# Kernel tuning notes

Measured on AMD Instinct MI355X. Metric: run time of the kernel, lower is better.

Reference implementation:

```python
import jax, jax.numpy as jnp
import numpy as np

N_NODES = 100000
N_EDGES = 1600000
HID = 128
N_GRAPHS = 512
MAX_Z = 1000
NODE_VOCAB = 200000
OUT = 2
BN_EPS = 1e-5


def setup_inputs() -> dict:
    key = jax.random.key(0)
    ks = jax.random.split(key, 20)

    def w(k, shape, fan_in):
        return jax.random.normal(k, shape, dtype=jnp.float32) / np.sqrt(fan_in)

    inp = {
        "num_nodes": N_NODES,
        "z": jax.random.randint(ks[0], (N_NODES,), 0, MAX_Z),
        "edge_index": jax.random.randint(ks[1], (2, N_EDGES), 0, N_NODES),
        "batch": jnp.sort(jax.random.randint(ks[2], (N_NODES,), 0, N_GRAPHS)),
        "node_id": jax.random.randint(ks[3], (N_NODES,), 0, NODE_VOCAB),
        # parameters
        "z_emb": jax.random.normal(ks[4], (MAX_Z, HID), dtype=jnp.float32) * 0.02,
        "node_emb": jax.random.normal(ks[5], (NODE_VOCAB, HID), dtype=jnp.float32) * 0.02,
        "W0": w(ks[6], (2 * HID, HID), 2 * HID), "b0": jnp.zeros((HID,), jnp.float32),
        "W1": w(ks[7], (HID, HID), HID), "b1": jnp.zeros((HID,), jnp.float32),
        "W2": w(ks[8], (HID, HID), HID), "b2": jnp.zeros((HID,), jnp.float32),
        "mlp_W1": w(ks[9], (HID, HID), HID), "mlp_b1": jnp.zeros((HID,), jnp.float32),
        "bn_gamma": jnp.ones((HID,), jnp.float32), "bn_beta": jnp.zeros((HID,), jnp.float32),
        "mlp_W2": w(ks[10], (HID, OUT), HID), "mlp_b2": jnp.zeros((OUT,), jnp.float32),
    }
    return inp


def _gin_conv(x, src, dst, W, b, num_nodes):
    # GINConv(eps=0): out_i = Linear(x_i + sum_{j->i} x_j)
    agg = jax.ops.segment_sum(x[src], dst, num_segments=num_nodes)
    return (x + agg) @ W + b


def reference(num_nodes, z, edge_index, batch, node_id,
              z_emb, node_emb, W0, b0, W1, b1, W2, b2,
              mlp_W1, mlp_b1, bn_gamma, bn_beta, mlp_W2, mlp_b2):
    src, dst = edge_index[0], edge_index[1]
    # node features: concat(z_embedding(z), node_embedding(node_id)) -> [N, 2H]
    x = jnp.concatenate([z_emb[z], node_emb[node_id]], axis=1)

    x = jax.nn.relu(_gin_conv(x, src, dst, W0, b0, num_nodes))  # [N, H]
    x = jax.nn.relu(_gin_conv(x, src, dst, W1, b1, num_nodes))
    x = _gin_conv(x, src, dst, W2, b2, num_nodes)  # last conv: no relu

    # global mean pool over graphs
    sums = jax.ops.segment_sum(x, batch, num_segments=N_GRAPHS)  # [G, H]
    counts = jax.ops.segment_sum(jnp.ones((num_nodes,), x.dtype), batch,
                                 num_segments=N_GRAPHS)
    pooled = sums / jnp.maximum(counts, 1.0)[:, None]

    # MLP([H, H, OUT]): Linear -> BatchNorm(eval, identity stats) -> ReLU -> Linear
    h = pooled @ mlp_W1 + mlp_b1
    h = h * (bn_gamma / np.sqrt(1.0 + BN_EPS)) + bn_beta
    h = jax.nn.relu(h)
    return h @ mlp_W2 + mlp_b2  # [G, OUT]
```

## Files before the change

kernel.cpp:

```cpp
#include <hip/hip_runtime.h>

#define NN 100000
#define NE 1600000
#define HID 128
#define NG 512
#define MAXZ 1000
#define NBK 256
#define BK_S 391
#define TILE_E 4096

typedef unsigned short u16;
typedef unsigned int u32;
typedef __attribute__((ext_vector_type(8))) short bf16x8;
typedef __attribute__((ext_vector_type(4))) float f32x4;

__device__ __forceinline__ u16 bf16r(float x) {
    u32 u = __float_as_uint(x);
    u32 r = (u + 0x7fffu + ((u >> 16) & 1u)) >> 16;
    return (u16)r;
}
__device__ __forceinline__ float bflo(u32 u) { return __uint_as_float(u << 16); }
__device__ __forceinline__ float bfhi(u32 u) { return __uint_as_float(u & 0xffff0000u); }

#define ACC8(v) { \
    acc[0] += bflo((v).x); acc[1] += bfhi((v).x); \
    acc[2] += bflo((v).y); acc[3] += bfhi((v).y); \
    acc[4] += bflo((v).z); acc[5] += bfhi((v).z); \
    acc[6] += bflo((v).w); acc[7] += bfhi((v).w); }

__global__ __launch_bounds__(256) void bucket_count_kernel(const int* __restrict__ dst,
                                                           int* __restrict__ bcount) {
    __shared__ int lh[NBK];
    int t = threadIdx.x;
    lh[t] = 0;
    __syncthreads();
    int stride = gridDim.x * 256;
    for (int i = blockIdx.x * 256 + t; i < NE; i += stride)
        atomicAdd(&lh[dst[i] / BK_S], 1);
    __syncthreads();
    int v = lh[t];
    if (v) atomicAdd(&bcount[t], v);
}

__global__ __launch_bounds__(NBK) void scan_nbk_kernel(const int* __restrict__ bcount,
                                                       int* __restrict__ boff,
                                                       int* __restrict__ gcursor) {
    __shared__ int buf[NBK];
    int t = threadIdx.x;
    int v = bcount[t];
    buf[t] = v;
    __syncthreads();
    for (int d = 1; d < NBK; d <<= 1) {
        int add = (t >= d) ? buf[t - d] : 0;
        __syncthreads();
        buf[t] += add;
        __syncthreads();
    }
    int excl = buf[t] - v;
    boff[t] = excl;
    gcursor[t] = excl;
    if (t == NBK - 1) boff[NBK] = buf[NBK - 1];
}

__global__ __launch_bounds__(256) void pair_scatter_kernel(const int* __restrict__ src,
                                                           const int* __restrict__ dst,
                                                           int* __restrict__ gcursor,
                                                           u32* __restrict__ pairs) {
    __shared__ int cnt[NBK];
    __shared__ int base[NBK];
    int t = threadIdx.x;
    long tile0 = (long)blockIdx.x * TILE_E;
    cnt[t] = 0;
    __syncthreads();
    u32 val[16], br[16];
#pragma unroll
    for (int i = 0; i < 16; ++i) {
        long idx = tile0 + i * 256 + t;
        val[i] = 0xFFFFFFFFu;
        if (idx < NE) {
            int d = dst[idx];
            int b = d / BK_S;
            int r = atomicAdd(&cnt[b], 1);
            val[i] = ((u32)(d - b * BK_S) << 17) | (u32)src[idx];
            br[i] = ((u32)b << 12) | (u32)r;
        }
    }
    __syncthreads();
    int c = cnt[t];
    if (c) base[t] = atomicAdd(&gcursor[t], c);
    __syncthreads();
#pragma unroll
    for (int i = 0; i < 16; ++i) {
        if (val[i] != 0xFFFFFFFFu) {
            u32 b = br[i] >> 12, r = br[i] & 0xFFFu;
            pairs[base[b] + r] = val[i];
        }
    }
}

__global__ __launch_bounds__(256) void bucket_build_kernel(const u32* __restrict__ pairs,
                                                           const int* __restrict__ boff,
                                                           int* __restrict__ off,
                                                           int* __restrict__ csr) {
    __shared__ int lh[BK_S];
    __shared__ int ts[256];
    int b = blockIdx.x, t = threadIdx.x;
    int base = boff[b], end = boff[b + 1];
    int node0 = b * BK_S;
    for (int i = t; i < BK_S; i += 256) lh[i] = 0;
    __syncthreads();
    for (int j = base + t; j < end; j += 256)
        atomicAdd(&lh[pairs[j] >> 17], 1);
    __syncthreads();
    int i0 = t * 2, i1 = t * 2 + 1;
    int c0 = (i0 < BK_S) ? lh[i0] : 0;
    int c1 = (i1 < BK_S) ? lh[i1] : 0;
    int s = c0 + c1;
    ts[t] = s;
    __syncthreads();
    for (int d = 1; d < 256; d <<= 1) {
        int add = (t >= d) ? ts[t - d] : 0;
        __syncthreads();
        ts[t] += add;
        __syncthreads();
    }
    int e0 = base + ts[t] - s;
    int e1 = e0 + c0;
    if (i0 < BK_S) { lh[i0] = e0; int n = node0 + i0; if (n < NN) off[n] = e0; }
    if (i1 < BK_S) { lh[i1] = e1; int n = node0 + i1; if (n < NN) off[n] = e1; }
    if (b == 0 && t == 0) off[NN] = NE;
    __syncthreads();
    for (int j = base + t; j < end; j += 256) {
        u32 p = pairs[j];
        int pos = atomicAdd(&lh[p >> 17], 1);
        csr[pos] = (int)(p & 0x1FFFFu);
    }
}

__global__ __launch_bounds__(128) void wt_kernel(const float* __restrict__ W, u16* __restrict__ Wt) {
    int k = blockIdx.x, n = threadIdx.x;
    Wt[n * HID + k] = bf16r(W[k * HID + n]);
}

#define FMA4(acc, s, w) { acc.x += (s)*(w).x; acc.y += (s)*(w).y; acc.z += (s)*(w).z; acc.w += (s)*(w).w; }
__global__ __launch_bounds__(256) void gemm128_kernel(
    const float* __restrict__ X, const float* __restrict__ W,
    float* __restrict__ Y, int nrows)
{
    __shared__ float xs[32][132];
    int t = threadIdx.x;
    int row0 = blockIdx.x * 32;
    int sr = t >> 5;
    int sk = (t & 31) * 4;
#pragma unroll
    for (int p = 0; p < 4; ++p) {
        int r = p * 8 + sr;
        int grow = row0 + r;
        float4 v = make_float4(0.f, 0.f, 0.f, 0.f);
        if (grow < nrows) v = *(const float4*)(X + (long)grow * HID + sk);
        *(float4*)(&xs[r][sk]) = v;
    }
    __syncthreads();
    int cg = t & 31, rg = t >> 5;
    int c = cg * 4, r = rg * 4;
    float4 a0 = make_float4(0,0,0,0), a1 = a0, a2 = a0, a3 = a0;
    for (int k = 0; k < 128; k += 4) {
        float x0[4], x1[4], x2[4], x3[4];
        *(float4*)x0 = *(const float4*)&xs[r + 0][k];
        *(float4*)x1 = *(const float4*)&xs[r + 1][k];
        *(float4*)x2 = *(const float4*)&xs[r + 2][k];
        *(float4*)x3 = *(const float4*)&xs[r + 3][k];
#pragma unroll
        for (int j = 0; j < 4; ++j) {
            float4 w = *(const float4*)(W + (k + j) * HID + c);
            FMA4(a0, x0[j], w); FMA4(a1, x1[j], w); FMA4(a2, x2[j], w); FMA4(a3, x3[j], w);
        }
    }
    float4 accs[4] = {a0, a1, a2, a3};
#pragma unroll
    for (int i = 0; i < 4; ++i) {
        int grow = row0 + r + i;
        if (grow < nrows) *(float4*)(Y + (long)grow * HID + c) = accs[i];
    }
}

template<int SRC_BF16>
__global__ __launch_bounds__(256) void mfma_gemm_kernel(
    const void* __restrict__ Xsrc,
    const int* __restrict__ gatherIdx,
    const u16* __restrict__ Wt,
    const float* __restrict__ addTab, const int* __restrict__ addIdx,
    u16* __restrict__ Y, int nrows)
{
    __shared__ u16 Als[64][136];
    __shared__ u16 Wls[128][136];
    int t = threadIdx.x;
    int row0 = blockIdx.x * 64;

#pragma unroll
    for (int p = 0; p < 2; ++p) {
        int n = p * 64 + (t >> 2);
        int k0 = (t & 3) * 32;
        const u16* src = Wt + n * HID + k0;
        uint4 v0 = *(const uint4*)(src);
        uint4 v1 = *(const uint4*)(src + 8);
        uint4 v2 = *(const uint4*)(src + 16);
        uint4 v3 = *(const uint4*)(src + 24);
        *(uint4*)&Wls[n][k0]      = v0;
        *(uint4*)&Wls[n][k0 + 8]  = v1;
        *(uint4*)&Wls[n][k0 + 16] = v2;
        *(uint4*)&Wls[n][k0 + 24] = v3;
    }

    if (SRC_BF16) {
        const u16* X = (const u16*)Xsrc;
#pragma unroll
        for (int p = 0; p < 4; ++p) {
            int r = p * 16 + (t >> 4);
            int k0 = (t & 15) * 8;
            int grow = row0 + r;
            uint4 v = make_uint4(0, 0, 0, 0);
            if (grow < nrows) {
                long srow = gatherIdx ? (long)gatherIdx[grow] : (long)grow;
                v = *(const uint4*)(X + srow * HID + k0);
            }
            *(uint4*)&Als[r][k0] = v;
        }
    } else {
        const float* X = (const float*)Xsrc;
#pragma unroll
        for (int p = 0; p < 8; ++p) {
            int r = p * 8 + (t >> 5);
            int k0 = (t & 31) * 4;
            int grow = row0 + r;
            float4 v = make_float4(0.f, 0.f, 0.f, 0.f);
            if (grow < nrows) {
                long srow = gatherIdx ? (long)gatherIdx[grow] : (long)grow;
                v = *(const float4*)(X + srow * HID + k0);
            }
            ushort4 b;
            b.x = bf16r(v.x); b.y = bf16r(v.y); b.z = bf16r(v.z); b.w = bf16r(v.w);
            *(ushort4*)&Als[r][k0] = b;
        }
    }
    __syncthreads();

    int w = t >> 6, l = t & 63;
    int lr = l & 15, lq = l >> 4;
    f32x4 acc[8];
#pragma unroll
    for (int i = 0; i < 8; ++i) acc[i] = (f32x4){0.f, 0.f, 0.f, 0.f};

#pragma unroll
    for (int kk = 0; kk < 4; ++kk) {
        bf16x8 af = *(const bf16x8*)&Als[w * 16 + lr][kk * 32 + lq * 8];
#pragma unroll
        for (int nt = 0; nt < 8; ++nt) {
            bf16x8 bf = *(const bf16x8*)&Wls[nt * 16 + lr][kk * 32 + lq * 8];
            acc[nt] = __builtin_amdgcn_mfma_f32_16x16x32_bf16(af, bf, acc[nt], 0, 0, 0);
        }
    }

    int orow = row0 + w * 16 + lq * 4;
#pragma unroll
    for (int r = 0; r < 4; ++r) {
        int grow = orow + r;
        if (grow < nrows) {
            const float* ap = addTab ? (addTab + (long)addIdx[grow] * HID) : nullptr;
#pragma unroll
            for (int nt = 0; nt < 8; ++nt) {
                int col = nt * 16 + lr;
                float v = acc[nt][r];
                if (ap) v += ap[col];
                Y[(long)grow * HID + col] = bf16r(v);
            }
        }
    }
}

__global__ __launch_bounds__(256) void aggregate_kernel(
    const u16* __restrict__ H, u16* __restrict__ Xo,
    const int* __restrict__ off, const int* __restrict__ csr,
    const float* __restrict__ bias, int n, int doRelu)
{
    int node = blockIdx.x * 4 + (threadIdx.x >> 6);
    if (node >= n) return;
    int lane = threadIdx.x & 63;
    int g = lane >> 4, fl = lane & 15;
    int s = off[node], e = off[node + 1];

    float acc[8] = {0.f, 0.f, 0.f, 0.f, 0.f, 0.f, 0.f, 0.f};
    int j = s + g;

    for (; j + 12 < e; j += 16) {
        int i0 = csr[j];
        int i1 = csr[j + 4];
        int i2 = csr[j + 8];
        int i3 = csr[j + 12];
        uint4 v0 = *(const uint4*)(H + (long)i0 * HID + fl * 8);
        uint4 v1 = *(const uint4*)(H + (long)i1 * HID + fl * 8);
        uint4 v2 = *(const uint4*)(H + (long)i2 * HID + fl * 8);
        uint4 v3 = *(const uint4*)(H + (long)i3 * HID + fl * 8);
        ACC8(v0); ACC8(v1); ACC8(v2); ACC8(v3);
    }
    for (; j + 4 < e; j += 8) {
        int i0 = csr[j];
        int i1 = csr[j + 4];
        uint4 v0 = *(const uint4*)(H + (long)i0 * HID + fl * 8);
        uint4 v1 = *(const uint4*)(H + (long)i1 * HID + fl * 8);
        ACC8(v0); ACC8(v1);
    }
    if (j < e) {
        int i0 = csr[j];
        uint4 v0 = *(const uint4*)(H + (long)i0 * HID + fl * 8);
        ACC8(v0);
    }

#pragma unroll
    for (int i = 0; i < 8; ++i) {
        acc[i] += __shfl_xor(acc[i], 16);
        acc[i] += __shfl_xor(acc[i], 32);
    }

    if (g == 0) {
        uint4 sv = *(const uint4*)(H + (long)node * HID + fl * 8);
        float4 ba = *(const float4*)(bias + fl * 8);
        float4 bb = *(const float4*)(bias + fl * 8 + 4);
        float r[8];
        r[0] = acc[0] + bflo(sv.x) + ba.x;
        r[1] = acc[1] + bfhi(sv.x) + ba.y;
        r[2] = acc[2] + bflo(sv.y) + ba.z;
        r[3] = acc[3] + bfhi(sv.y) + ba.w;
        r[4] = acc[4] + bflo(sv.z) + bb.x;
        r[5] = acc[5] + bfhi(sv.z) + bb.y;
        r[6] = acc[6] + bflo(sv.w) + bb.z;
        r[7] = acc[7] + bfhi(sv.w) + bb.w;
        if (doRelu) {
#pragma unroll
            for (int i = 0; i < 8; ++i) r[i] = fmaxf(r[i], 0.f);
        }
        uint4 ov;
        ov.x = (u32)bf16r(r[0]) | ((u32)bf16r(r[1]) << 16);
        ov.y = (u32)bf16r(r[2]) | ((u32)bf16r(r[3]) << 16);
        ov.z = (u32)bf16r(r[4]) | ((u32)bf16r(r[5]) << 16);
        ov.w = (u32)bf16r(r[6]) | ((u32)bf16r(r[7]) << 16);
        *(uint4*)(Xo + (long)node * HID + fl * 8) = ov;
    }
}

__global__ __launch_bounds__(256) void pool_kernel(const u16* __restrict__ X, const int* __restrict__ batch,
                                                   int n, float* __restrict__ pooled) {
    __shared__ float red[4][HID];
    int g = blockIdx.x;
    int t = threadIdx.x;
    int grp = t >> 4, fl = t & 15;
    int lo = 0, hi = n;
    while (lo < hi) { int m = (lo + hi) >> 1; if (batch[m] < g) lo = m + 1; else hi = m; }
    int s = lo;
    lo = 0; hi = n;
    while (lo < hi) { int m = (lo + hi) >> 1; if (batch[m] < g + 1) lo = m + 1; else hi = m; }
    int e = lo;

    float acc[8] = {0.f, 0.f, 0.f, 0.f, 0.f, 0.f, 0.f, 0.f};
    for (int i = s + grp; i < e; i += 16) {
        uint4 v = *(const uint4*)(X + (long)i * HID + fl * 8);
        ACC8(v);
    }
#pragma unroll
    for (int i = 0; i < 8; ++i) {
        acc[i] += __shfl_xor(acc[i], 16);
        acc[i] += __shfl_xor(acc[i], 32);
    }
    int w = t >> 6, lane = t & 63;
    if (lane < 16) {
#pragma unroll
        for (int i = 0; i < 8; ++i) red[w][lane * 8 + i] = acc[i];
    }
    __syncthreads();
    if (t < HID) {
        float v = red[0][t] + red[1][t] + red[2][t] + red[3][t];
        float cnt = (float)(e - s);
        pooled[g * HID + t] = v / fmaxf(cnt, 1.f);
    }
}

__global__ __launch_bounds__(128) void mlp_kernel(
    const float* __restrict__ pooled, const float* __restrict__ W1, const float* __restrict__ b1,
    const float* __restrict__ gamma, const float* __restrict__ beta,
    const float* __restrict__ W2, const float* __restrict__ b2, float* __restrict__ out)
{
    int g = blockIdx.x, t = threadIdx.x;
    __shared__ float p[HID];
    __shared__ float red[4];
    p[t] = pooled[g * HID + t];
    __syncthreads();
    float acc = b1[t];
    for (int k = 0; k < HID; ++k) acc += p[k] * W1[k * HID + t];
    const float inv = 1.0f / sqrtf(1.0f + 1e-5f);
    acc = acc * (gamma[t] * inv) + beta[t];
    acc = fmaxf(acc, 0.f);
    float v0 = acc * W2[t * 2 + 0];
    float v1 = acc * W2[t * 2 + 1];
    for (int d = 32; d > 0; d >>= 1) { v0 += __shfl_down(v0, d); v1 += __shfl_down(v1, d); }
    int w = t >> 6, lane = t & 63;
    if (lane == 0) { red[w * 2] = v0; red[w * 2 + 1] = v1; }
    __syncthreads();
    if (t == 0) {
        out[g * 2 + 0] = red[0] + red[2] + b2[0];
        out[g * 2 + 1] = red[1] + red[3] + b2[1];
    }
}

extern "C" void kernel_launch(void* const* d_in, const int* in_sizes, int n_in,
                              void* d_out, int out_size, void* d_ws, size_t ws_size,
                              hipStream_t stream) {
    const int*   z        = (const int*)d_in[1];
    const int*   ei       = (const int*)d_in[2];
    const int*   batch    = (const int*)d_in[3];
    const int*   node_id  = (const int*)d_in[4];
    const float* z_emb    = (const float*)d_in[5];
    const float* node_emb = (const float*)d_in[6];
    const float* W0  = (const float*)d_in[7];
    const float* b0  = (const float*)d_in[8];
    const float* W1  = (const float*)d_in[9];
    const float* b1  = (const float*)d_in[10];
    const float* W2  = (const float*)d_in[11];
    const float* b2  = (const float*)d_in[12];
    const float* mW1 = (const float*)d_in[13];
    const float* mb1 = (const float*)d_in[14];
    const float* gam = (const float*)d_in[15];
    const float* bet = (const float*)d_in[16];
    const float* mW2 = (const float*)d_in[17];
    const float* mb2 = (const float*)d_in[18];
    float* out = (float*)d_out;

    const int* srcArr = ei;
    const int* dstArr = ei + NE;

    char* ws = (char*)d_ws;
    size_t o = 0;
    auto alloc = [&](size_t bytes) { char* p = ws + o; o += (bytes + 255) & ~(size_t)255; return p; };
    u16*   A      = (u16*)alloc((size_t)NN * HID * 2);
    u16*   B      = (u16*)alloc((size_t)NN * HID * 2);
    float* zW     = (float*)alloc((size_t)MAXZ * HID * 4);
    u16*   W0bt   = (u16*)alloc((size_t)HID * HID * 2);
    u16*   W1t    = (u16*)alloc((size_t)HID * HID * 2);
    u16*   W2t    = (u16*)alloc((size_t)HID * HID * 2);
    int*   bcount = (int*)alloc((size_t)NBK * 4);
    int*   boff   = (int*)alloc((size_t)(NBK + 1) * 4);
    int*   gcur   = (int*)alloc((size_t)NBK * 4);
    u32*   pairs  = (u32*)alloc((size_t)NE * 4);
    int*   off    = (int*)alloc((size_t)(NN + 1) * 4);
    int*   csr    = (int*)alloc((size_t)NE * 4);
    float* pooled = (float*)alloc((size_t)NG * HID * 4);
    (void)ws_size;

    hipMemsetAsync(bcount, 0, (size_t)NBK * 4, stream);
    bucket_count_kernel<<<1024, 256, 0, stream>>>(dstArr, bcount);
    scan_nbk_kernel<<<1, NBK, 0, stream>>>(bcount, boff, gcur);
    pair_scatter_kernel<<<(NE + TILE_E - 1) / TILE_E, 256, 0, stream>>>(srcArr, dstArr, gcur, pairs);
    bucket_build_kernel<<<NBK, 256, 0, stream>>>(pairs, boff, off, csr);

    wt_kernel<<<HID, HID, 0, stream>>>(W0 + HID * HID, W0bt);
    wt_kernel<<<HID, HID, 0, stream>>>(W1, W1t);
    wt_kernel<<<HID, HID, 0, stream>>>(W2, W2t);

    gemm128_kernel<<<(MAXZ + 31) / 32, 256, 0, stream>>>(z_emb, W0, zW, MAXZ);

    const int GB = (NN + 63) / 64;
    mfma_gemm_kernel<0><<<GB, 256, 0, stream>>>(node_emb, node_id, W0bt, zW, z, B, NN);
    aggregate_kernel<<<NN / 4, 256, 0, stream>>>(B, A, off, csr, b0, NN, 1);
    mfma_gemm_kernel<1><<<GB, 256, 0, stream>>>(A, nullptr, W1t, nullptr, nullptr, B, NN);
    aggregate_kernel<<<NN / 4, 256, 0, stream>>>(B, A, off, csr, b1, NN, 1);
    mfma_gemm_kernel<1><<<GB, 256, 0, stream>>>(A, nullptr, W2t, nullptr, nullptr, B, NN);
    aggregate_kernel<<<NN / 4, 256, 0, stream>>>(B, A, off, csr, b2, NN, 0);

    pool_kernel<<<NG, 256, 0, stream>>>(A, batch, NN, pooled);
    mlp_kernel<<<NG, 128, 0, stream>>>(pooled, mW1, mb1, gam, bet, mW2, mb2, out);
}
```

Before: 377.9 us.

## Defer last GIN linear layer past mean pooling by linearity

The last GIN conv has no ReLU and feeds a linear mean pool, so the W2 matmul and b2 bias are moved after pooling and applied to the 512 pooled rows inside the MLP kernel. This removes a full 100k-row MFMA GEMM and its feature-matrix round trip. The final aggregation now runs without bias on the layer-2 activations, and the weight transposes merge into a single launch. Pooling happens before the bf16 rounding of the W2 output, so the numerics change slightly.

```diff
diff --git a/kernel.cpp b/kernel.cpp
--- a/kernel.cpp
+++ b/kernel.cpp
@@ -137,9 +137,14 @@
     }
 }
 
-__global__ __launch_bounds__(128) void wt_kernel(const float* __restrict__ W, u16* __restrict__ Wt) {
-    int k = blockIdx.x, n = threadIdx.x;
-    Wt[n * HID + k] = bf16r(W[k * HID + n]);
+__global__ __launch_bounds__(128) void wt2_kernel(const float* __restrict__ W0b, const float* __restrict__ W1,
+                                                  u16* __restrict__ W0bt, u16* __restrict__ W1t) {
+    int k = blockIdx.x & 127;
+    int which = blockIdx.x >> 7;
+    int n = threadIdx.x;
+    const float* W = which ? W1 : W0b;
+    u16* o = which ? W1t : W0bt;
+    o[n * HID + k] = bf16r(W[k * HID + n]);
 }
 
 #define FMA4(acc, s, w) { acc.x += (s)*(w).x; acc.y += (s)*(w).y; acc.z += (s)*(w).z; acc.w += (s)*(w).w; }
@@ -324,17 +329,21 @@
 
     if (g == 0) {
         uint4 sv = *(const uint4*)(H + (long)node * HID + fl * 8);
-        float4 ba = *(const float4*)(bias + fl * 8);
-        float4 bb = *(const float4*)(bias + fl * 8 + 4);
         float r[8];
-        r[0] = acc[0] + bflo(sv.x) + ba.x;
-        r[1] = acc[1] + bfhi(sv.x) + ba.y;
-        r[2] = acc[2] + bflo(sv.y) + ba.z;
-        r[3] = acc[3] + bfhi(sv.y) + ba.w;
-        r[4] = acc[4] + bflo(sv.z) + bb.x;
-        r[5] = acc[5] + bfhi(sv.z) + bb.y;
-        r[6] = acc[6] + bflo(sv.w) + bb.z;
-        r[7] = acc[7] + bfhi(sv.w) + bb.w;
+        r[0] = acc[0] + bflo(sv.x);
+        r[1] = acc[1] + bfhi(sv.x);
+        r[2] = acc[2] + bflo(sv.y);
+        r[3] = acc[3] + bfhi(sv.y);
+        r[4] = acc[4] + bflo(sv.z);
+        r[5] = acc[5] + bfhi(sv.z);
+        r[6] = acc[6] + bflo(sv.w);
+        r[7] = acc[7] + bfhi(sv.w);
+        if (bias) {
+            float4 ba = *(const float4*)(bias + fl * 8);
+            float4 bb = *(const float4*)(bias + fl * 8 + 4);
+            r[0] += ba.x; r[1] += ba.y; r[2] += ba.z; r[3] += ba.w;
+            r[4] += bb.x; r[5] += bb.y; r[6] += bb.z; r[7] += bb.w;
+        }
         if (doRelu) {
 #pragma unroll
             for (int i = 0; i < 8; ++i) r[i] = fmaxf(r[i], 0.f);
@@ -385,29 +394,35 @@
 }
 
 __global__ __launch_bounds__(128) void mlp_kernel(
-    const float* __restrict__ pooled, const float* __restrict__ W1, const float* __restrict__ b1,
+    const float* __restrict__ poolT, const float* __restrict__ W2f, const float* __restrict__ b2,
+    const float* __restrict__ W1, const float* __restrict__ b1,
     const float* __restrict__ gamma, const float* __restrict__ beta,
-    const float* __restrict__ W2, const float* __restrict__ b2, float* __restrict__ out)
+    const float* __restrict__ mW2, const float* __restrict__ mb2, float* __restrict__ out)
 {
     int g = blockIdx.x, t = threadIdx.x;
+    __shared__ float pt[HID];
     __shared__ float p[HID];
     __shared__ float red[4];
-    p[t] = pooled[g * HID + t];
+    pt[t] = poolT[g * HID + t];
+    __syncthreads();
+    float pv = b2[t];
+    for (int k = 0; k < HID; ++k) pv += pt[k] * W2f[k * HID + t];
+    p[t] = pv;
     __syncthreads();
     float acc = b1[t];
     for (int k = 0; k < HID; ++k) acc += p[k] * W1[k * HID + t];
     const float inv = 1.0f / sqrtf(1.0f + 1e-5f);
     acc = acc * (gamma[t] * inv) + beta[t];
     acc = fmaxf(acc, 0.f);
-    float v0 = acc * W2[t * 2 + 0];
-    float v1 = acc * W2[t * 2 + 1];
+    float v0 = acc * mW2[t * 2 + 0];
+    float v1 = acc * mW2[t * 2 + 1];
     for (int d = 32; d > 0; d >>= 1) { v0 += __shfl_down(v0, d); v1 += __shfl_down(v1, d); }
     int w = t >> 6, lane = t & 63;
     if (lane == 0) { red[w * 2] = v0; red[w * 2 + 1] = v1; }
     __syncthreads();
     if (t == 0) {
-        out[g * 2 + 0] = red[0] + red[2] + b2[0];
-        out[g * 2 + 1] = red[1] + red[3] + b2[1];
+        out[g * 2 + 0] = red[0] + red[2] + mb2[0];
+        out[g * 2 + 1] = red[1] + red[3] + mb2[1];
     }
 }
 
@@ -445,14 +460,13 @@
     float* zW     = (float*)alloc((size_t)MAXZ * HID * 4);
     u16*   W0bt   = (u16*)alloc((size_t)HID * HID * 2);
     u16*   W1t    = (u16*)alloc((size_t)HID * HID * 2);
-    u16*   W2t    = (u16*)alloc((size_t)HID * HID * 2);
     int*   bcount = (int*)alloc((size_t)NBK * 4);
     int*   boff   = (int*)alloc((size_t)(NBK + 1) * 4);
     int*   gcur   = (int*)alloc((size_t)NBK * 4);
     u32*   pairs  = (u32*)alloc((size_t)NE * 4);
     int*   off    = (int*)alloc((size_t)(NN + 1) * 4);
     int*   csr    = (int*)alloc((size_t)NE * 4);
-    float* pooled = (float*)alloc((size_t)NG * HID * 4);
+    float* poolT  = (float*)alloc((size_t)NG * HID * 4);
     (void)ws_size;
 
     hipMemsetAsync(bcount, 0, (size_t)NBK * 4, stream);
@@ -461,9 +475,7 @@
     pair_scatter_kernel<<<(NE + TILE_E - 1) / TILE_E, 256, 0, stream>>>(srcArr, dstArr, gcur, pairs);
     bucket_build_kernel<<<NBK, 256, 0, stream>>>(pairs, boff, off, csr);
 
-    wt_kernel<<<HID, HID, 0, stream>>>(W0 + HID * HID, W0bt);
-    wt_kernel<<<HID, HID, 0, stream>>>(W1, W1t);
-    wt_kernel<<<HID, HID, 0, stream>>>(W2, W2t);
+    wt2_kernel<<<2 * HID, HID, 0, stream>>>(W0 + HID * HID, W1, W0bt, W1t);
 
     gemm128_kernel<<<(MAXZ + 31) / 32, 256, 0, stream>>>(z_emb, W0, zW, MAXZ);
 
@@ -472,9 +484,8 @@
     aggregate_kernel<<<NN / 4, 256, 0, stream>>>(B, A, off, csr, b0, NN, 1);
     mfma_gemm_kernel<1><<<GB, 256, 0, stream>>>(A, nullptr, W1t, nullptr, nullptr, B, NN);
     aggregate_kernel<<<NN / 4, 256, 0, stream>>>(B, A, off, csr, b1, NN, 1);
-    mfma_gemm_kernel<1><<<GB, 256, 0, stream>>>(A, nullptr, W2t, nullptr, nullptr, B, NN);
-    aggregate_kernel<<<NN / 4, 256, 0, stream>>>(B, A, off, csr, b2, NN, 0);
-
-    pool_kernel<<<NG, 256, 0, stream>>>(A, batch, NN, pooled);
-    mlp_kernel<<<NG, 128, 0, stream>>>(pooled, mW1, mb1, gam, bet, mW2, mb2, out);
-}
+    aggregate_kernel<<<NN / 4, 256, 0, stream>>>(A, B, off, csr, nullptr, NN, 0);
+
+    pool_kernel<<<NG, 256, 0, stream>>>(B, batch, NN, poolT);
+    mlp_kernel<<<NG, 128, 0, stream>>>(poolT, W2, b2, mW1, mb1, gam, bet, mW2, mb2, out);
+}
```

Result: faster. 361.7 us (-4.3%).
